# Optimization experiments

Measured on AMD Instinct MI355X. Metric: run time of the kernel, lower is better.

Reference implementation:

```python
import jax, jax.numpy as jnp
import numpy as np

SIZE, D, DLOC, NUM_LABELS = 784, 32, 2, 10
LABEL_SITE = SIZE // 2
INIT_STD = 0.01


def tree_contract(mats):
    # mats: [n, B, D, D]; binary-tree pairwise matmul matching the torch loop
    # (odd level: last matrix set aside, re-appended after the pairwise bmm)
    n = mats.shape[0]
    while n > 1:
        if n % 2 == 1:
            lone = mats[-1:]
            mats = mats[:-1]
        else:
            lone = None
        mats = jnp.einsum('nbij,nbjk->nbik', mats[0::2], mats[1::2])
        if lone is not None:
            mats = jnp.concatenate([mats, lone], axis=0)
        n = mats.shape[0]
    return mats[0]  # [B, D, D]


def setup_inputs() -> dict:
    key = jax.random.key(0)
    k1, k2, k3 = jax.random.split(key, 3)
    batch_input = jax.random.uniform(k1, (128, SIZE), dtype=jnp.float32)
    # 'random_eye' init: identity (broadcast over site / physical / label dims) + noise
    core_tensors = (jnp.broadcast_to(jnp.eye(D, dtype=jnp.float32)[None, :, :, None],
                                     (SIZE, D, D, DLOC))
                    + INIT_STD * jax.random.normal(k2, (SIZE, D, D, DLOC), dtype=jnp.float32))
    label_tensor = (jnp.broadcast_to(jnp.eye(D, dtype=jnp.float32)[:, :, None],
                                     (D, D, NUM_LABELS))
                    + INIT_STD * jax.random.normal(k3, (D, D, NUM_LABELS), dtype=jnp.float32))
    return {"batch_input": batch_input, "core_tensors": core_tensors,
            "label_tensor": label_tensor}


def reference(batch_input, core_tensors, label_tensor):
    # embed: x -> [1-x, x], shape [B, S, d]
    embedded = jnp.stack([1.0 - batch_input, batch_input], axis=-1)
    # contract each core with its local feature vector -> [S, B, D, D]
    batch_mats = jnp.einsum('sijd,bsd->sbij', core_tensors, embedded)
    left = tree_contract(batch_mats[:LABEL_SITE])    # [B, D, D]
    right = tree_contract(batch_mats[LABEL_SITE:])   # [B, D, D]
    # trace(left @ label_l @ right) per batch and label -> [B, num_labels]
    scores = jnp.einsum('bij,jkl,bki->bl', left, label_tensor, right)
    return scores
```

## Files before the change

### kernel.cpp

```cpp
#include <hip/hip_runtime.h>
#include <cstddef>


typedef short bfrag __attribute__((ext_vector_type(4)));
typedef float facc  __attribute__((ext_vector_type(4)));

#if !defined(__HIP_DEVICE_COMPILE__)
#define MFMA16(a, b, c) (c)
#elif __has_builtin(__builtin_amdgcn_mfma_f32_16x16x16bf16_1k)
#define MFMA16(a, b, c) __builtin_amdgcn_mfma_f32_16x16x16bf16_1k(a, b, c, 0, 0, 0)
#elif __has_builtin(__builtin_amdgcn_mfma_f32_16x16x16_bf16)
#define MFMA16(a, b, c) __builtin_amdgcn_mfma_f32_16x16x16_bf16(a, b, c, 0, 0, 0)
#else
#error "no 16x16x16 bf16 MFMA builtin on this target"
#endif

#define CORE2B_DWORDS (784 * 1024)

__device__ __forceinline__ short bf16h(float v) {
  unsigned u = __float_as_uint(v) + 0x8000u;
  return (short)(u >> 16);
}

#if defined(__HIP_DEVICE_COMPILE__) && __has_builtin(__builtin_amdgcn_cvt_pk_bf16_f32)
typedef __bf16 bf16x2 __attribute__((ext_vector_type(2)));
__device__ __forceinline__ bfrag packf4(float a, float b, float c, float d) {
  bf16x2 lo = __builtin_amdgcn_cvt_pk_bf16_f32(a, b);
  bf16x2 hi = __builtin_amdgcn_cvt_pk_bf16_f32(c, d);
  uint2 u = make_uint2(__builtin_bit_cast(unsigned, lo), __builtin_bit_cast(unsigned, hi));
  return __builtin_bit_cast(bfrag, u);
}
#else
__device__ __forceinline__ bfrag packf4(float a, float b, float c, float d) {
  bfrag r; r[0] = bf16h(a); r[1] = bf16h(b); r[2] = bf16h(c); r[3] = bf16h(d);
  return r;
}
#endif

__device__ __forceinline__ bfrag pack4(const facc v) {
  return packf4(v[0], v[1], v[2], v[3]);
}

__device__ __forceinline__ void split4(const float* v, bfrag& hi, bfrag& lo) {
#pragma unroll
  for (int j = 0; j < 4; ++j) {
    unsigned u = (__float_as_uint(v[j]) + 0x8000u) & 0xFFFF0000u;
    hi[j] = (short)(u >> 16);
    float lf = v[j] - __uint_as_float(u);
    lo[j] = bf16h(lf);
  }
}

__device__ __forceinline__ void fold_step(facc (&acc)[2][2], const float4 (&av)[2][2]) {
  bfrag Ahi[2][2], Alo[2][2], Bhi[2][2], Blo[2][2];
#pragma unroll
  for (int R = 0; R < 2; ++R)
#pragma unroll
    for (int H = 0; H < 2; ++H) {
      float v[4] = {av[R][H].x, av[R][H].y, av[R][H].z, av[R][H].w};
      split4(v, Ahi[R][H], Alo[R][H]);
    }
#pragma unroll
  for (int H = 0; H < 2; ++H)
#pragma unroll
    for (int c = 0; c < 2; ++c) {
      float v[4] = {acc[H][c][0], acc[H][c][1], acc[H][c][2], acc[H][c][3]};
      split4(v, Bhi[H][c], Blo[H][c]);
    }
  facc n[2][2];
#pragma unroll
  for (int R = 0; R < 2; ++R)
#pragma unroll
    for (int c = 0; c < 2; ++c) {
      facc z;
#pragma unroll
      for (int j = 0; j < 4; ++j) z[j] = 0.0f;
#pragma unroll
      for (int H = 0; H < 2; ++H) {
        z = MFMA16(Ahi[R][H], Bhi[H][c], z);
        z = MFMA16(Ahi[R][H], Blo[H][c], z);
        z = MFMA16(Alo[R][H], Bhi[H][c], z);
      }
      n[R][c] = z;
    }
#pragma unroll
  for (int R = 0; R < 2; ++R)
#pragma unroll
    for (int c = 0; c < 2; ++c) acc[R][c] = n[R][c];
}

__global__ __launch_bounds__(256) void xform_k(const float* __restrict__ core,
                                               unsigned* __restrict__ core2b) {
  const int s = blockIdx.x;
  const int tid = threadIdx.x;
  const float4* src = (const float4*)(core + (size_t)s * 2048);
  unsigned* dst = core2b + (size_t)s * 1024;
#pragma unroll
  for (int u = 0; u < 2; ++u) {
    int v = tid + 256 * u;
    float4 f = src[v];
    int i = v >> 4;
    int c = (v & 15) * 2;
    int r = i >> 4, col16 = i & 15;
    int h2 = c >> 4, cl = c & 15;
    int q = cl >> 2, j = cl & 3;
    float e0a = f.x - ((i == c) ? 1.0f : 0.0f);
    float e0b = f.z - ((i == c + 1) ? 1.0f : 0.0f);
    unsigned wa = ((unsigned)(unsigned short)bf16h(f.y - f.x) << 16) |
                  (unsigned)(unsigned short)bf16h(e0a);
    unsigned wb = ((unsigned)(unsigned short)bf16h(f.w - f.z) << 16) |
                  (unsigned)(unsigned short)bf16h(e0b);
    int idx = ((r * 2 + h2) * 64 + 16 * q + col16) * 4 + j;
    *(uint2*)(dst + idx) = make_uint2(wa, wb);
  }
}

__global__ __launch_bounds__(512, 4) void kchain(const float* __restrict__ x,
                                                 const unsigned* __restrict__ core2b,
                                                 float* __restrict__ halfbuf) {
  const int tid = threadIdx.x;
  const int lane = tid & 63;
  const int k = tid >> 6;
  const int col16 = lane & 15;
  const int q = lane >> 4;

  const int bid = blockIdx.x;
  const int chain = bid >> 1;
  const int half = bid & 1;
  const int b = chain >> 1;
  const int hside = chain & 1;

  const int t = half * 8 + k;
  const int start = (t < 8) ? 25 * t : 200 + 24 * (t - 8);
  const int len = (t < 8) ? 25 : 24;
  const int s_lo = hside * 392 + start;
  const int s_hi = s_lo + len - 1;

  __shared__ float smX[8][32 * 36];

  facc acc[2][2];
#pragma unroll
  for (int r = 0; r < 2; ++r)
#pragma unroll
    for (int c = 0; c < 2; ++c)
#pragma unroll
      for (int j = 0; j < 4; ++j)
        acc[r][c][j] = (16 * r + 4 * q + j == 16 * c + col16) ? 1.0f : 0.0f;

  const uint4* cp = (const uint4*)core2b;
  const float* xb = x + b * 784;

  for (int s = s_hi; s >= s_lo; --s) {
    uint4 raw[4];
#pragma unroll
    for (int f = 0; f < 4; ++f) raw[f] = cp[(size_t)s * 256 + f * 64 + lane];
    const float xv = xb[s];

    bfrag B[2][2];
#pragma unroll
    for (int h2 = 0; h2 < 2; ++h2)
#pragma unroll
      for (int c = 0; c < 2; ++c) B[h2][c] = pack4(acc[h2][c]);

    bfrag A[2][2];
#pragma unroll
    for (int r = 0; r < 2; ++r)
#pragma unroll
      for (int h2 = 0; h2 < 2; ++h2) {
        unsigned wd[4] = {raw[r * 2 + h2].x, raw[r * 2 + h2].y, raw[r * 2 + h2].z,
                          raw[r * 2 + h2].w};
        float e[4];
#pragma unroll
        for (int j = 0; j < 4; ++j) {
          float e0 = __uint_as_float(wd[j] << 16);
          float d = __uint_as_float(wd[j] & 0xFFFF0000u);
          e[j] = fmaf(xv, d, e0);
        }
        A[r][h2] = packf4(e[0], e[1], e[2], e[3]);
      }

#pragma unroll
    for (int r = 0; r < 2; ++r)
#pragma unroll
      for (int c = 0; c < 2; ++c) {
        acc[r][c] = MFMA16(A[r][0], B[0][c], acc[r][c]);
        acc[r][c] = MFMA16(A[r][1], B[1][c], acc[r][c]);
      }
  }

#pragma unroll
  for (int r = 0; r < 2; ++r)
#pragma unroll
    for (int c = 0; c < 2; ++c)
      *(float4*)&smX[k][(16 * c + col16) * 36 + 16 * r + 4 * q] =
          make_float4(acc[r][c][0], acc[r][c][1], acc[r][c][2], acc[r][c][3]);
  __syncthreads();

  facc a2[2][2];
#pragma unroll
  for (int r = 0; r < 2; ++r)
#pragma unroll
    for (int c = 0; c < 2; ++c)
#pragma unroll
      for (int j = 0; j < 4; ++j)
        a2[r][c][j] = (16 * r + 4 * q + j == 16 * c + col16) ? 1.0f : 0.0f;

  const int fo0 = (16 * 0 + col16) * 36 + 4 * q;
  const int fo1 = (16 * 1 + col16) * 36 + 4 * q;

  if ((k & 1) == 0) {
    float4 av[2][2];
#pragma unroll
    for (int R = 0; R < 2; ++R)
#pragma unroll
      for (int H = 0; H < 2; ++H)
        av[R][H] = *(const float4*)&smX[k][(R ? fo1 : fo0) + 16 * H];
    fold_step(a2, av);
#pragma unroll
    for (int R = 0; R < 2; ++R)
#pragma unroll
      for (int H = 0; H < 2; ++H)
        av[R][H] = *(const float4*)&smX[k + 1][(R ? fo1 : fo0) + 16 * H];
    fold_step(a2, av);
  }
  __syncthreads();
  if (k == 2 || k == 6) {
#pragma unroll
    for (int r = 0; r < 2; ++r)
#pragma unroll
      for (int c = 0; c < 2; ++c)
#pragma unroll
        for (int j = 0; j < 4; ++j)
          smX[k][(16 * r + 4 * q + j) * 36 + 16 * c + col16] = a2[r][c][j];
  }
  __syncthreads();
  if (k == 0 || k == 4) {
    float4 av[2][2];
#pragma unroll
    for (int R = 0; R < 2; ++R)
#pragma unroll
      for (int H = 0; H < 2; ++H)
        av[R][H] = *(const float4*)&smX[k + 2][(R ? fo1 : fo0) + 16 * H];
    fold_step(a2, av);
  }
  __syncthreads();
  if (k == 4) {
#pragma unroll
    for (int r = 0; r < 2; ++r)
#pragma unroll
      for (int c = 0; c < 2; ++c)
#pragma unroll
        for (int j = 0; j < 4; ++j)
          smX[4][(16 * r + 4 * q + j) * 36 + 16 * c + col16] = a2[r][c][j];
  }
  __syncthreads();
  if (k == 0) {
    float4 av[2][2];
#pragma unroll
    for (int R = 0; R < 2; ++R)
#pragma unroll
      for (int H = 0; H < 2; ++H)
        av[R][H] = *(const float4*)&smX[4][(R ? fo1 : fo0) + 16 * H];
    fold_step(a2, av);
    float* rm = halfbuf + (size_t)bid * 1024;
#pragma unroll
    for (int r = 0; r < 2; ++r)
#pragma unroll
      for (int c = 0; c < 2; ++c)
#pragma unroll
        for (int j = 0; j < 4; ++j)
          rm[(16 * r + 4 * q + j) * 32 + 16 * c + col16] = a2[r][c][j];
  }
}

__global__ __launch_bounds__(64) void gfin(const float* __restrict__ halfbuf,
                                           const float* __restrict__ label,
                                           float* __restrict__ out) {
  const int lane = threadIdx.x;
  const int b = blockIdx.x;
  const int col16 = lane & 15;
  const int q = lane >> 4;

  __shared__ float smF[1024];

  facc acc[2][2];
#pragma unroll
  for (int r = 0; r < 2; ++r)
#pragma unroll
    for (int c = 0; c < 2; ++c)
#pragma unroll
      for (int j = 0; j < 4; ++j)
        acc[r][c][j] = (16 * r + 4 * q + j == 16 * c + col16) ? 1.0f : 0.0f;

  const int slots[4] = {(2 * b + 1) * 2 + 0, (2 * b + 1) * 2 + 1,
                        (2 * b) * 2 + 0, (2 * b) * 2 + 1};
#pragma unroll
  for (int m = 0; m < 4; ++m) {
    const float* rm = halfbuf + (size_t)slots[m] * 1024;
    float4 av[2][2];
#pragma unroll
    for (int R = 0; R < 2; ++R)
#pragma unroll
      for (int H = 0; H < 2; ++H)
        av[R][H] = *(const float4*)&rm[(16 * R + col16) * 32 + 16 * H + 4 * q];
    fold_step(acc, av);
  }

#pragma unroll
  for (int r = 0; r < 2; ++r)
#pragma unroll
    for (int c = 0; c < 2; ++c)
#pragma unroll
      for (int j = 0; j < 4; ++j)
        smF[(16 * r + 4 * q + j) * 32 + 16 * c + col16] = acc[r][c][j];
  __syncthreads();

  float part[10];
#pragma unroll
  for (int l = 0; l < 10; ++l) part[l] = 0.0f;
#pragma unroll
  for (int u = 0; u < 16; ++u) {
    int e = lane + 64 * u;
    float v = smF[e];
    const float* lb = label + (size_t)e * 10;
#pragma unroll
    for (int l = 0; l < 10; ++l) part[l] += v * lb[l];
  }
#pragma unroll
  for (int l = 0; l < 10; ++l) {
#pragma unroll
    for (int o = 32; o > 0; o >>= 1) part[l] += __shfl_xor(part[l], o, 64);
  }
  if (lane == 0) {
#pragma unroll
    for (int l = 0; l < 10; ++l) out[b * 10 + l] = part[l];
  }
}

extern "C" void kernel_launch(void* const* d_in, const int* in_sizes, int n_in,
                              void* d_out, int out_size, void* d_ws, size_t ws_size,
                              hipStream_t stream) {
  const float* x = (const float*)d_in[0];
  const float* core = (const float*)d_in[1];
  const float* label = (const float*)d_in[2];
  float* out = (float*)d_out;

  unsigned* core2b = (unsigned*)d_ws;
  float* halfbuf = (float*)d_ws + CORE2B_DWORDS;

  hipLaunchKernelGGL(xform_k, dim3(784), dim3(256), 0, stream, core, core2b);
  hipLaunchKernelGGL(kchain, dim3(512), dim3(512), 0, stream, x, core2b, halfbuf);
  hipLaunchKernelGGL(gfin, dim3(128), dim3(64), 0, stream, halfbuf, label, out);
}
```

Before: 93.25 us.

## Split core matrix into E0 and D MFMA terms, scale B by x instead

The per-site matrix A = E0 + x*D is no longer rebuilt per element. The kernel issues two MFMAs per tile, one with E0 against B and one with D against x*B, so the per-element unpack, FMA and repack work on the A side is removed at the cost of twice the MFMA count. The transform kernel lays out the E0 and D halves as separate bf16 fragments, and x values are loaded once per lane and broadcast by shuffle instead of a scalar load each step. Launch bounds are raised to allow 8 blocks per CU, which may pressure registers. Rounding changes slightly because x*B is rounded to bf16.

```diff
diff --git a/kernel.cpp b/kernel.cpp
--- a/kernel.cpp
+++ b/kernel.cpp
@@ -37,10 +37,6 @@
 }
 #endif
 
-__device__ __forceinline__ bfrag pack4(const facc v) {
-  return packf4(v[0], v[1], v[2], v[3]);
-}
-
 __device__ __forceinline__ void split4(const float* v, bfrag& hi, bfrag& lo) {
 #pragma unroll
   for (int j = 0; j < 4; ++j) {
@@ -104,18 +100,20 @@
     int r = i >> 4, col16 = i & 15;
     int h2 = c >> 4, cl = c & 15;
     int q = cl >> 2, j = cl & 3;
+    int lane = col16 + 16 * q;
+    int slot = (r * 2 + h2) * 64 + lane;
     float e0a = f.x - ((i == c) ? 1.0f : 0.0f);
     float e0b = f.z - ((i == c + 1) ? 1.0f : 0.0f);
-    unsigned wa = ((unsigned)(unsigned short)bf16h(f.y - f.x) << 16) |
-                  (unsigned)(unsigned short)bf16h(e0a);
-    unsigned wb = ((unsigned)(unsigned short)bf16h(f.w - f.z) << 16) |
-                  (unsigned)(unsigned short)bf16h(e0b);
-    int idx = ((r * 2 + h2) * 64 + 16 * q + col16) * 4 + j;
-    *(uint2*)(dst + idx) = make_uint2(wa, wb);
-  }
-}
-
-__global__ __launch_bounds__(512, 4) void kchain(const float* __restrict__ x,
+    unsigned e0pair = ((unsigned)(unsigned short)bf16h(e0b) << 16) |
+                      (unsigned)(unsigned short)bf16h(e0a);
+    unsigned dpair = ((unsigned)(unsigned short)bf16h(f.w - f.z) << 16) |
+                     (unsigned)(unsigned short)bf16h(f.y - f.x);
+    dst[4 * slot + (j >> 1)] = e0pair;
+    dst[4 * slot + 2 + (j >> 1)] = dpair;
+  }
+}
+
+__global__ __launch_bounds__(512, 8) void kchain(const float* __restrict__ x,
                                                  const unsigned* __restrict__ core2b,
                                                  float* __restrict__ halfbuf) {
   const int tid = threadIdx.x;
@@ -150,41 +148,36 @@
   const uint4* cp = (const uint4*)core2b;
   const float* xb = x + b * 784;
 
+  float xr = (lane < len) ? xb[s_lo + lane] : 0.0f;
+
   for (int s = s_hi; s >= s_lo; --s) {
     uint4 raw[4];
 #pragma unroll
     for (int f = 0; f < 4; ++f) raw[f] = cp[(size_t)s * 256 + f * 64 + lane];
-    const float xv = xb[s];
-
-    bfrag B[2][2];
+    const float xv = __shfl(xr, s - s_lo, 64);
+
+    bfrag B[2][2], Bx[2][2];
 #pragma unroll
     for (int h2 = 0; h2 < 2; ++h2)
 #pragma unroll
-      for (int c = 0; c < 2; ++c) B[h2][c] = pack4(acc[h2][c]);
-
-    bfrag A[2][2];
+      for (int c = 0; c < 2; ++c) {
+        facc a = acc[h2][c];
+        B[h2][c] = packf4(a[0], a[1], a[2], a[3]);
+        Bx[h2][c] = packf4(xv * a[0], xv * a[1], xv * a[2], xv * a[3]);
+      }
+
 #pragma unroll
     for (int r = 0; r < 2; ++r)
 #pragma unroll
       for (int h2 = 0; h2 < 2; ++h2) {
-        unsigned wd[4] = {raw[r * 2 + h2].x, raw[r * 2 + h2].y, raw[r * 2 + h2].z,
-                          raw[r * 2 + h2].w};
-        float e[4];
-#pragma unroll
-        for (int j = 0; j < 4; ++j) {
-          float e0 = __uint_as_float(wd[j] << 16);
-          float d = __uint_as_float(wd[j] & 0xFFFF0000u);
-          e[j] = fmaf(xv, d, e0);
+        const uint4 rw = raw[r * 2 + h2];
+        bfrag E0 = __builtin_bit_cast(bfrag, make_uint2(rw.x, rw.y));
+        bfrag Dd = __builtin_bit_cast(bfrag, make_uint2(rw.z, rw.w));
+#pragma unroll
+        for (int c = 0; c < 2; ++c) {
+          acc[r][c] = MFMA16(Dd, Bx[h2][c], acc[r][c]);
+          acc[r][c] = MFMA16(E0, B[h2][c], acc[r][c]);
         }
-        A[r][h2] = packf4(e[0], e[1], e[2], e[3]);
-      }
-
-#pragma unroll
-    for (int r = 0; r < 2; ++r)
-#pragma unroll
-      for (int c = 0; c < 2; ++c) {
-        acc[r][c] = MFMA16(A[r][0], B[0][c], acc[r][c]);
-        acc[r][c] = MFMA16(A[r][1], B[1][c], acc[r][c]);
       }
   }
 
```

After: 97.85 us. +4.9%, slower.

## Fuse three kernels into one persistent kernel with grid barrier and last-block finalize

Applied to the files above, without the earlier changes.

Merges the core-transform, chain-contraction and final-trace kernels into one launch. A global atomic counter acts as a grid-wide barrier between the transform phase and the chain phase. A per-batch atomic counter lets the last of the four finishing blocks do the label contraction. This removes two kernel launch gaps and the separate final pass. The cost is a memset launch plus spin-waiting, and the barrier can deadlock if the 512 blocks cannot all be resident at once; a bounded guard mitigates this but may silently break correctness.

```diff
diff --git a/kernel.cpp b/kernel.cpp
--- a/kernel.cpp
+++ b/kernel.cpp
@@ -15,7 +15,16 @@
 #error "no 16x16x16 bf16 MFMA builtin on this target"
 #endif
 
+#if defined(__HIP_DEVICE_COMPILE__)
+#define S_SLEEP() __builtin_amdgcn_s_sleep(2)
+#else
+#define S_SLEEP()
+#endif
+
 #define CORE2B_DWORDS (784 * 1024)
+#define HALF_FLOATS (512 * 1024)
+#define CTR_DWORD_OFF (CORE2B_DWORDS + HALF_FLOATS)
+#define NBLK 512u
 
 __device__ __forceinline__ short bf16h(float v) {
   unsigned u = __float_as_uint(v) + 0x8000u;
@@ -89,251 +98,263 @@
     for (int c = 0; c < 2; ++c) acc[R][c] = n[R][c];
 }
 
-__global__ __launch_bounds__(256) void xform_k(const float* __restrict__ core,
-                                               unsigned* __restrict__ core2b) {
-  const int s = blockIdx.x;
+__global__ __launch_bounds__(512, 4) void fused_k(const float* __restrict__ x,
+                                                  const float* __restrict__ core,
+                                                  const float* __restrict__ label,
+                                                  unsigned* __restrict__ core2b,
+                                                  float* __restrict__ halfbuf,
+                                                  unsigned* __restrict__ ctrs,
+                                                  float* __restrict__ out) {
   const int tid = threadIdx.x;
-  const float4* src = (const float4*)(core + (size_t)s * 2048);
-  unsigned* dst = core2b + (size_t)s * 1024;
-#pragma unroll
-  for (int u = 0; u < 2; ++u) {
-    int v = tid + 256 * u;
-    float4 f = src[v];
-    int i = v >> 4;
-    int c = (v & 15) * 2;
-    int r = i >> 4, col16 = i & 15;
-    int h2 = c >> 4, cl = c & 15;
-    int q = cl >> 2, j = cl & 3;
-    float e0a = f.x - ((i == c) ? 1.0f : 0.0f);
-    float e0b = f.z - ((i == c + 1) ? 1.0f : 0.0f);
-    unsigned wa = ((unsigned)(unsigned short)bf16h(f.y - f.x) << 16) |
-                  (unsigned)(unsigned short)bf16h(e0a);
-    unsigned wb = ((unsigned)(unsigned short)bf16h(f.w - f.z) << 16) |
-                  (unsigned)(unsigned short)bf16h(e0b);
-    int idx = ((r * 2 + h2) * 64 + 16 * q + col16) * 4 + j;
-    *(uint2*)(dst + idx) = make_uint2(wa, wb);
+  const int bid = blockIdx.x;
+  __shared__ float smX[8][32 * 36];
+
+  {
+    const int gtid = bid * 512 + tid;
+    for (int idx = gtid; idx < 784 * 512; idx += 512 * 512) {
+      const int s = idx >> 9;
+      const int v = idx & 511;
+      const float4 f = ((const float4*)(core + (size_t)s * 2048))[v];
+      unsigned* dst = core2b + (size_t)s * 1024;
+      int i = v >> 4;
+      int c = (v & 15) * 2;
+      int r = i >> 4, col16 = i & 15;
+      int h2 = c >> 4, cl = c & 15;
+      int q = cl >> 2, j = cl & 3;
+      float e0a = f.x - ((i == c) ? 1.0f : 0.0f);
+      float e0b = f.z - ((i == c + 1) ? 1.0f : 0.0f);
+      unsigned wa = ((unsigned)(unsigned short)bf16h(f.y - f.x) << 16) |
+                    (unsigned)(unsigned short)bf16h(e0a);
+      unsigned wb = ((unsigned)(unsigned short)bf16h(f.w - f.z) << 16) |
+                    (unsigned)(unsigned short)bf16h(e0b);
+      int di = ((r * 2 + h2) * 64 + 16 * q + col16) * 4 + j;
+      *(uint2*)(dst + di) = make_uint2(wa, wb);
+    }
   }
-}
-
-__global__ __launch_bounds__(512, 4) void kchain(const float* __restrict__ x,
-                                                 const unsigned* __restrict__ core2b,
-                                                 float* __restrict__ halfbuf) {
-  const int tid = threadIdx.x;
-  const int lane = tid & 63;
-  const int k = tid >> 6;
-  const int col16 = lane & 15;
-  const int q = lane >> 4;
-
-  const int bid = blockIdx.x;
-  const int chain = bid >> 1;
-  const int half = bid & 1;
-  const int b = chain >> 1;
-  const int hside = chain & 1;
-
-  const int t = half * 8 + k;
-  const int start = (t < 8) ? 25 * t : 200 + 24 * (t - 8);
-  const int len = (t < 8) ? 25 : 24;
-  const int s_lo = hside * 392 + start;
-  const int s_hi = s_lo + len - 1;
-
-  __shared__ float smX[8][32 * 36];
-
-  facc acc[2][2];
-#pragma unroll
-  for (int r = 0; r < 2; ++r)
-#pragma unroll
-    for (int c = 0; c < 2; ++c)
-#pragma unroll
-      for (int j = 0; j < 4; ++j)
-        acc[r][c][j] = (16 * r + 4 * q + j == 16 * c + col16) ? 1.0f : 0.0f;
-
-  const uint4* cp = (const uint4*)core2b;
-  const float* xb = x + b * 784;
-
-  for (int s = s_hi; s >= s_lo; --s) {
-    uint4 raw[4];
-#pragma unroll
-    for (int f = 0; f < 4; ++f) raw[f] = cp[(size_t)s * 256 + f * 64 + lane];
-    const float xv = xb[s];
-
-    bfrag B[2][2];
-#pragma unroll
-    for (int h2 = 0; h2 < 2; ++h2)
-#pragma unroll
-      for (int c = 0; c < 2; ++c) B[h2][c] = pack4(acc[h2][c]);
-
-    bfrag A[2][2];
-#pragma unroll
-    for (int r = 0; r < 2; ++r)
-#pragma unroll
-      for (int h2 = 0; h2 < 2; ++h2) {
-        unsigned wd[4] = {raw[r * 2 + h2].x, raw[r * 2 + h2].y, raw[r * 2 + h2].z,
-                          raw[r * 2 + h2].w};
-        float e[4];
-#pragma unroll
-        for (int j = 0; j < 4; ++j) {
-          float e0 = __uint_as_float(wd[j] << 16);
-          float d = __uint_as_float(wd[j] & 0xFFFF0000u);
-          e[j] = fmaf(xv, d, e0);
-        }
-        A[r][h2] = packf4(e[0], e[1], e[2], e[3]);
-      }
-
-#pragma unroll
-    for (int r = 0; r < 2; ++r)
-#pragma unroll
-      for (int c = 0; c < 2; ++c) {
-        acc[r][c] = MFMA16(A[r][0], B[0][c], acc[r][c]);
-        acc[r][c] = MFMA16(A[r][1], B[1][c], acc[r][c]);
-      }
-  }
-
-#pragma unroll
-  for (int r = 0; r < 2; ++r)
-#pragma unroll
-    for (int c = 0; c < 2; ++c)
-      *(float4*)&smX[k][(16 * c + col16) * 36 + 16 * r + 4 * q] =
-          make_float4(acc[r][c][0], acc[r][c][1], acc[r][c][2], acc[r][c][3]);
+
+  __threadfence();
   __syncthreads();
-
-  facc a2[2][2];
-#pragma unroll
-  for (int r = 0; r < 2; ++r)
-#pragma unroll
-    for (int c = 0; c < 2; ++c)
-#pragma unroll
-      for (int j = 0; j < 4; ++j)
-        a2[r][c][j] = (16 * r + 4 * q + j == 16 * c + col16) ? 1.0f : 0.0f;
-
-  const int fo0 = (16 * 0 + col16) * 36 + 4 * q;
-  const int fo1 = (16 * 1 + col16) * 36 + 4 * q;
-
-  if ((k & 1) == 0) {
-    float4 av[2][2];
-#pragma unroll
-    for (int R = 0; R < 2; ++R)
-#pragma unroll
-      for (int H = 0; H < 2; ++H)
-        av[R][H] = *(const float4*)&smX[k][(R ? fo1 : fo0) + 16 * H];
-    fold_step(a2, av);
-#pragma unroll
-    for (int R = 0; R < 2; ++R)
-#pragma unroll
-      for (int H = 0; H < 2; ++H)
-        av[R][H] = *(const float4*)&smX[k + 1][(R ? fo1 : fo0) + 16 * H];
-    fold_step(a2, av);
+  if (tid == 0) {
+    __hip_atomic_fetch_add(&ctrs[0], 1u, __ATOMIC_ACQ_REL, __HIP_MEMORY_SCOPE_AGENT);
+    int guard = 0;
+    while (__hip_atomic_load(&ctrs[0], __ATOMIC_RELAXED, __HIP_MEMORY_SCOPE_AGENT) <
+           NBLK) {
+      S_SLEEP();
+      if (++guard > (1 << 22)) break;
+    }
   }
   __syncthreads();
-  if (k == 2 || k == 6) {
+  __threadfence();
+
+  {
+    const int lane = tid & 63;
+    const int k = tid >> 6;
+    const int col16 = lane & 15;
+    const int q = lane >> 4;
+
+    const int chain = bid >> 1;
+    const int half = bid & 1;
+    const int b = chain >> 1;
+    const int hside = chain & 1;
+
+    const int t = half * 8 + k;
+    const int start = (t < 8) ? 25 * t : 200 + 24 * (t - 8);
+    const int len = (t < 8) ? 25 : 24;
+    const int s_lo = hside * 392 + start;
+    const int s_hi = s_lo + len - 1;
+
+    facc acc[2][2];
 #pragma unroll
     for (int r = 0; r < 2; ++r)
 #pragma unroll
       for (int c = 0; c < 2; ++c)
 #pragma unroll
         for (int j = 0; j < 4; ++j)
-          smX[k][(16 * r + 4 * q + j) * 36 + 16 * c + col16] = a2[r][c][j];
-  }
-  __syncthreads();
-  if (k == 0 || k == 4) {
-    float4 av[2][2];
-#pragma unroll
-    for (int R = 0; R < 2; ++R)
-#pragma unroll
-      for (int H = 0; H < 2; ++H)
-        av[R][H] = *(const float4*)&smX[k + 2][(R ? fo1 : fo0) + 16 * H];
-    fold_step(a2, av);
-  }
-  __syncthreads();
-  if (k == 4) {
+          acc[r][c][j] = (16 * r + 4 * q + j == 16 * c + col16) ? 1.0f : 0.0f;
+
+    const uint4* cp = (const uint4*)core2b;
+    const float* xb = x + b * 784;
+
+    for (int s = s_hi; s >= s_lo; --s) {
+      uint4 raw[4];
+#pragma unroll
+      for (int f = 0; f < 4; ++f) raw[f] = cp[(size_t)s * 256 + f * 64 + lane];
+      const float xv = xb[s];
+
+      bfrag B[2][2];
+#pragma unroll
+      for (int h2 = 0; h2 < 2; ++h2)
+#pragma unroll
+        for (int c = 0; c < 2; ++c) B[h2][c] = pack4(acc[h2][c]);
+
+      bfrag A[2][2];
+#pragma unroll
+      for (int r = 0; r < 2; ++r)
+#pragma unroll
+        for (int h2 = 0; h2 < 2; ++h2) {
+          unsigned wd[4] = {raw[r * 2 + h2].x, raw[r * 2 + h2].y, raw[r * 2 + h2].z,
+                            raw[r * 2 + h2].w};
+          float e[4];
+#pragma unroll
+          for (int j = 0; j < 4; ++j) {
+            float e0 = __uint_as_float(wd[j] << 16);
+            float d = __uint_as_float(wd[j] & 0xFFFF0000u);
+            e[j] = fmaf(xv, d, e0);
+          }
+          A[r][h2] = packf4(e[0], e[1], e[2], e[3]);
+        }
+
+#pragma unroll
+      for (int r = 0; r < 2; ++r)
+#pragma unroll
+        for (int c = 0; c < 2; ++c) {
+          acc[r][c] = MFMA16(A[r][0], B[0][c], acc[r][c]);
+          acc[r][c] = MFMA16(A[r][1], B[1][c], acc[r][c]);
+        }
+    }
+
 #pragma unroll
     for (int r = 0; r < 2; ++r)
 #pragma unroll
       for (int c = 0; c < 2; ++c)
+        *(float4*)&smX[k][(16 * c + col16) * 36 + 16 * r + 4 * q] =
+            make_float4(acc[r][c][0], acc[r][c][1], acc[r][c][2], acc[r][c][3]);
+    __syncthreads();
+
+    facc a2[2][2];
+#pragma unroll
+    for (int r = 0; r < 2; ++r)
+#pragma unroll
+      for (int c = 0; c < 2; ++c)
 #pragma unroll
         for (int j = 0; j < 4; ++j)
-          smX[4][(16 * r + 4 * q + j) * 36 + 16 * c + col16] = a2[r][c][j];
-  }
-  __syncthreads();
-  if (k == 0) {
-    float4 av[2][2];
-#pragma unroll
-    for (int R = 0; R < 2; ++R)
-#pragma unroll
-      for (int H = 0; H < 2; ++H)
-        av[R][H] = *(const float4*)&smX[4][(R ? fo1 : fo0) + 16 * H];
-    fold_step(a2, av);
-    float* rm = halfbuf + (size_t)bid * 1024;
-#pragma unroll
-    for (int r = 0; r < 2; ++r)
-#pragma unroll
-      for (int c = 0; c < 2; ++c)
-#pragma unroll
-        for (int j = 0; j < 4; ++j)
-          rm[(16 * r + 4 * q + j) * 32 + 16 * c + col16] = a2[r][c][j];
-  }
-}
-
-__global__ __launch_bounds__(64) void gfin(const float* __restrict__ halfbuf,
-                                           const float* __restrict__ label,
-                                           float* __restrict__ out) {
-  const int lane = threadIdx.x;
-  const int b = blockIdx.x;
-  const int col16 = lane & 15;
-  const int q = lane >> 4;
-
-  __shared__ float smF[1024];
-
-  facc acc[2][2];
-#pragma unroll
-  for (int r = 0; r < 2; ++r)
-#pragma unroll
-    for (int c = 0; c < 2; ++c)
-#pragma unroll
-      for (int j = 0; j < 4; ++j)
-        acc[r][c][j] = (16 * r + 4 * q + j == 16 * c + col16) ? 1.0f : 0.0f;
-
-  const int slots[4] = {(2 * b + 1) * 2 + 0, (2 * b + 1) * 2 + 1,
-                        (2 * b) * 2 + 0, (2 * b) * 2 + 1};
-#pragma unroll
-  for (int m = 0; m < 4; ++m) {
-    const float* rm = halfbuf + (size_t)slots[m] * 1024;
-    float4 av[2][2];
-#pragma unroll
-    for (int R = 0; R < 2; ++R)
-#pragma unroll
-      for (int H = 0; H < 2; ++H)
-        av[R][H] = *(const float4*)&rm[(16 * R + col16) * 32 + 16 * H + 4 * q];
-    fold_step(acc, av);
-  }
-
-#pragma unroll
-  for (int r = 0; r < 2; ++r)
-#pragma unroll
-    for (int c = 0; c < 2; ++c)
-#pragma unroll
-      for (int j = 0; j < 4; ++j)
-        smF[(16 * r + 4 * q + j) * 32 + 16 * c + col16] = acc[r][c][j];
-  __syncthreads();
-
-  float part[10];
-#pragma unroll
-  for (int l = 0; l < 10; ++l) part[l] = 0.0f;
-#pragma unroll
-  for (int u = 0; u < 16; ++u) {
-    int e = lane + 64 * u;
-    float v = smF[e];
-    const float* lb = label + (size_t)e * 10;
-#pragma unroll
-    for (int l = 0; l < 10; ++l) part[l] += v * lb[l];
-  }
-#pragma unroll
-  for (int l = 0; l < 10; ++l) {
-#pragma unroll
-    for (int o = 32; o > 0; o >>= 1) part[l] += __shfl_xor(part[l], o, 64);
-  }
-  if (lane == 0) {
-#pragma unroll
-    for (int l = 0; l < 10; ++l) out[b * 10 + l] = part[l];
+          a2[r][c][j] = (16 * r + 4 * q + j == 16 * c + col16) ? 1.0f : 0.0f;
+
+    const int fo0 = (16 * 0 + col16) * 36 + 4 * q;
+    const int fo1 = (16 * 1 + col16) * 36 + 4 * q;
+
+    if ((k & 1) == 0) {
+      float4 av[2][2];
+#pragma unroll
+      for (int R = 0; R < 2; ++R)
+#pragma unroll
+        for (int H = 0; H < 2; ++H)
+          av[R][H] = *(const float4*)&smX[k][(R ? fo1 : fo0) + 16 * H];
+      fold_step(a2, av);
+#pragma unroll
+      for (int R = 0; R < 2; ++R)
+#pragma unroll
+        for (int H = 0; H < 2; ++H)
+          av[R][H] = *(const float4*)&smX[k + 1][(R ? fo1 : fo0) + 16 * H];
+      fold_step(a2, av);
+    }
+    __syncthreads();
+    if (k == 2 || k == 6) {
+#pragma unroll
+      for (int r = 0; r < 2; ++r)
+#pragma unroll
+        for (int c = 0; c < 2; ++c)
+#pragma unroll
+          for (int j = 0; j < 4; ++j)
+            smX[k][(16 * r + 4 * q + j) * 36 + 16 * c + col16] = a2[r][c][j];
+    }
+    __syncthreads();
+    if (k == 0 || k == 4) {
+      float4 av[2][2];
+#pragma unroll
+      for (int R = 0; R < 2; ++R)
+#pragma unroll
+        for (int H = 0; H < 2; ++H)
+          av[R][H] = *(const float4*)&smX[k + 2][(R ? fo1 : fo0) + 16 * H];
+      fold_step(a2, av);
+    }
+    __syncthreads();
+    if (k == 4) {
+#pragma unroll
+      for (int r = 0; r < 2; ++r)
+#pragma unroll
+        for (int c = 0; c < 2; ++c)
+#pragma unroll
+          for (int j = 0; j < 4; ++j)
+            smX[4][(16 * r + 4 * q + j) * 36 + 16 * c + col16] = a2[r][c][j];
+    }
+    __syncthreads();
+    if (k == 0) {
+      float4 av[2][2];
+#pragma unroll
+      for (int R = 0; R < 2; ++R)
+#pragma unroll
+        for (int H = 0; H < 2; ++H)
+          av[R][H] = *(const float4*)&smX[4][(R ? fo1 : fo0) + 16 * H];
+      fold_step(a2, av);
+      float* rm = halfbuf + (size_t)bid * 1024;
+#pragma unroll
+      for (int r = 0; r < 2; ++r)
+#pragma unroll
+        for (int c = 0; c < 2; ++c)
+#pragma unroll
+          for (int j = 0; j < 4; ++j)
+            rm[(16 * r + 4 * q + j) * 32 + 16 * c + col16] = a2[r][c][j];
+
+      __threadfence();
+      unsigned old = 0;
+      if (lane == 0)
+        old = __hip_atomic_fetch_add(&ctrs[1 + b], 1u, __ATOMIC_ACQ_REL,
+                                     __HIP_MEMORY_SCOPE_AGENT);
+      old = __shfl(old, 0, 64);
+      if (old == 3u) {
+        __threadfence();
+
+        facc hacc[2][2];
+#pragma unroll
+        for (int r = 0; r < 2; ++r)
+#pragma unroll
+          for (int c = 0; c < 2; ++c)
+#pragma unroll
+            for (int j = 0; j < 4; ++j)
+              hacc[r][c][j] = (16 * r + 4 * q + j == 16 * c + col16) ? 1.0f : 0.0f;
+
+        const int slots[4] = {(2 * b + 1) * 2 + 0, (2 * b + 1) * 2 + 1,
+                              (2 * b) * 2 + 0, (2 * b) * 2 + 1};
+#pragma unroll
+        for (int m = 0; m < 4; ++m) {
+          const float* rm2 = halfbuf + (size_t)slots[m] * 1024;
+          float4 qv[2][2];
+#pragma unroll
+          for (int R = 0; R < 2; ++R)
+#pragma unroll
+            for (int H = 0; H < 2; ++H)
+              qv[R][H] =
+                  *(const float4*)&rm2[(16 * R + col16) * 32 + 16 * H + 4 * q];
+          fold_step(hacc, qv);
+        }
+
+        float part[10];
+#pragma unroll
+        for (int l = 0; l < 10; ++l) part[l] = 0.0f;
+#pragma unroll
+        for (int r = 0; r < 2; ++r)
+#pragma unroll
+          for (int c = 0; c < 2; ++c)
+#pragma unroll
+            for (int j = 0; j < 4; ++j) {
+              float v = hacc[r][c][j];
+              const float* lb =
+                  label + (size_t)((16 * r + 4 * q + j) * 32 + 16 * c + col16) * 10;
+#pragma unroll
+              for (int l = 0; l < 10; ++l) part[l] += v * lb[l];
+            }
+#pragma unroll
+        for (int l = 0; l < 10; ++l) {
+#pragma unroll
+          for (int o = 32; o > 0; o >>= 1) part[l] += __shfl_xor(part[l], o, 64);
+        }
+        if (lane == 0) {
+#pragma unroll
+          for (int l = 0; l < 10; ++l) out[b * 10 + l] = part[l];
+        }
+      }
+    }
   }
 }
 
@@ -347,8 +368,9 @@
 
   unsigned* core2b = (unsigned*)d_ws;
   float* halfbuf = (float*)d_ws + CORE2B_DWORDS;
-
-  hipLaunchKernelGGL(xform_k, dim3(784), dim3(256), 0, stream, core, core2b);
-  hipLaunchKernelGGL(kchain, dim3(512), dim3(512), 0, stream, x, core2b, halfbuf);
-  hipLaunchKernelGGL(gfin, dim3(128), dim3(64), 0, stream, halfbuf, label, out);
-}
+  unsigned* ctrs = (unsigned*)d_ws + CTR_DWORD_OFF;
+
+  hipMemsetAsync(ctrs, 0, (1 + 128) * sizeof(unsigned), stream);
+  hipLaunchKernelGGL(fused_k, dim3(512), dim3(512), 0, stream, x, core, label,
+                     core2b, halfbuf, ctrs, out);
+}
```

New measurement: 284.1 us. 3.05x slower.

## Fuse final label contraction into chain kernel via last-block atomic counter

Applied to the files above, without the earlier changes.

Removes the separate gfin kernel launch. Each kchain block bumps a per-batch atomic counter after writing its half-chain matrix, and the fourth block to arrive folds the four partial matrices and contracts the result with the label tensor in registers. This removes one kernel launch and its dependency gap. In exchange it adds a memset launch, threadfences, and a serial tail on the last-arriving blocks.

```diff
diff --git a/kernel.cpp b/kernel.cpp
--- a/kernel.cpp
+++ b/kernel.cpp
@@ -16,6 +16,8 @@
 #endif
 
 #define CORE2B_DWORDS (784 * 1024)
+#define HALF_FLOATS (512 * 1024)
+#define CTR_DWORD_OFF (CORE2B_DWORDS + HALF_FLOATS)
 
 __device__ __forceinline__ short bf16h(float v) {
   unsigned u = __float_as_uint(v) + 0x8000u;
@@ -117,7 +119,10 @@
 
 __global__ __launch_bounds__(512, 4) void kchain(const float* __restrict__ x,
                                                  const unsigned* __restrict__ core2b,
-                                                 float* __restrict__ halfbuf) {
+                                                 float* __restrict__ halfbuf,
+                                                 unsigned* __restrict__ ctrs,
+                                                 const float* __restrict__ label,
+                                                 float* __restrict__ out) {
   const int tid = threadIdx.x;
   const int lane = tid & 63;
   const int k = tid >> 6;
@@ -270,70 +275,64 @@
 #pragma unroll
         for (int j = 0; j < 4; ++j)
           rm[(16 * r + 4 * q + j) * 32 + 16 * c + col16] = a2[r][c][j];
-  }
-}
-
-__global__ __launch_bounds__(64) void gfin(const float* __restrict__ halfbuf,
-                                           const float* __restrict__ label,
-                                           float* __restrict__ out) {
-  const int lane = threadIdx.x;
-  const int b = blockIdx.x;
-  const int col16 = lane & 15;
-  const int q = lane >> 4;
-
-  __shared__ float smF[1024];
-
-  facc acc[2][2];
-#pragma unroll
-  for (int r = 0; r < 2; ++r)
-#pragma unroll
-    for (int c = 0; c < 2; ++c)
-#pragma unroll
-      for (int j = 0; j < 4; ++j)
-        acc[r][c][j] = (16 * r + 4 * q + j == 16 * c + col16) ? 1.0f : 0.0f;
-
-  const int slots[4] = {(2 * b + 1) * 2 + 0, (2 * b + 1) * 2 + 1,
-                        (2 * b) * 2 + 0, (2 * b) * 2 + 1};
-#pragma unroll
-  for (int m = 0; m < 4; ++m) {
-    const float* rm = halfbuf + (size_t)slots[m] * 1024;
-    float4 av[2][2];
-#pragma unroll
-    for (int R = 0; R < 2; ++R)
-#pragma unroll
-      for (int H = 0; H < 2; ++H)
-        av[R][H] = *(const float4*)&rm[(16 * R + col16) * 32 + 16 * H + 4 * q];
-    fold_step(acc, av);
-  }
-
-#pragma unroll
-  for (int r = 0; r < 2; ++r)
-#pragma unroll
-    for (int c = 0; c < 2; ++c)
-#pragma unroll
-      for (int j = 0; j < 4; ++j)
-        smF[(16 * r + 4 * q + j) * 32 + 16 * c + col16] = acc[r][c][j];
-  __syncthreads();
-
-  float part[10];
-#pragma unroll
-  for (int l = 0; l < 10; ++l) part[l] = 0.0f;
-#pragma unroll
-  for (int u = 0; u < 16; ++u) {
-    int e = lane + 64 * u;
-    float v = smF[e];
-    const float* lb = label + (size_t)e * 10;
-#pragma unroll
-    for (int l = 0; l < 10; ++l) part[l] += v * lb[l];
-  }
-#pragma unroll
-  for (int l = 0; l < 10; ++l) {
-#pragma unroll
-    for (int o = 32; o > 0; o >>= 1) part[l] += __shfl_xor(part[l], o, 64);
-  }
-  if (lane == 0) {
-#pragma unroll
-    for (int l = 0; l < 10; ++l) out[b * 10 + l] = part[l];
+
+    __threadfence();
+    unsigned old = 0;
+    if (lane == 0)
+      old = __hip_atomic_fetch_add(&ctrs[b], 1u, __ATOMIC_ACQ_REL,
+                                   __HIP_MEMORY_SCOPE_AGENT);
+    old = __shfl(old, 0, 64);
+    if (old == 3u) {
+      __threadfence();
+
+      facc hacc[2][2];
+#pragma unroll
+      for (int r = 0; r < 2; ++r)
+#pragma unroll
+        for (int c = 0; c < 2; ++c)
+#pragma unroll
+          for (int j = 0; j < 4; ++j)
+            hacc[r][c][j] = (16 * r + 4 * q + j == 16 * c + col16) ? 1.0f : 0.0f;
+
+      const int slots[4] = {(2 * b + 1) * 2 + 0, (2 * b + 1) * 2 + 1,
+                            (2 * b) * 2 + 0, (2 * b) * 2 + 1};
+#pragma unroll
+      for (int m = 0; m < 4; ++m) {
+        const float* rm2 = halfbuf + (size_t)slots[m] * 1024;
+        float4 qv[2][2];
+#pragma unroll
+        for (int R = 0; R < 2; ++R)
+#pragma unroll
+          for (int H = 0; H < 2; ++H)
+            qv[R][H] = *(const float4*)&rm2[(16 * R + col16) * 32 + 16 * H + 4 * q];
+        fold_step(hacc, qv);
+      }
+
+      float part[10];
+#pragma unroll
+      for (int l = 0; l < 10; ++l) part[l] = 0.0f;
+#pragma unroll
+      for (int r = 0; r < 2; ++r)
+#pragma unroll
+        for (int c = 0; c < 2; ++c)
+#pragma unroll
+          for (int j = 0; j < 4; ++j) {
+            float v = hacc[r][c][j];
+            const float* lb =
+                label + (size_t)((16 * r + 4 * q + j) * 32 + 16 * c + col16) * 10;
+#pragma unroll
+            for (int l = 0; l < 10; ++l) part[l] += v * lb[l];
+          }
+#pragma unroll
+      for (int l = 0; l < 10; ++l) {
+#pragma unroll
+        for (int o = 32; o > 0; o >>= 1) part[l] += __shfl_xor(part[l], o, 64);
+      }
+      if (lane == 0) {
+#pragma unroll
+        for (int l = 0; l < 10; ++l) out[b * 10 + l] = part[l];
+      }
+    }
   }
 }
 
@@ -347,8 +346,10 @@
 
   unsigned* core2b = (unsigned*)d_ws;
   float* halfbuf = (float*)d_ws + CORE2B_DWORDS;
-
+  unsigned* ctrs = (unsigned*)d_ws + CTR_DWORD_OFF;
+
+  hipMemsetAsync(ctrs, 0, 128 * sizeof(unsigned), stream);
   hipLaunchKernelGGL(xform_k, dim3(784), dim3(256), 0, stream, core, core2b);
-  hipLaunchKernelGGL(kchain, dim3(512), dim3(512), 0, stream, x, core2b, halfbuf);
-  hipLaunchKernelGGL(gfin, dim3(128), dim3(64), 0, stream, halfbuf, label, out);
-}
+  hipLaunchKernelGGL(kchain, dim3(512), dim3(512), 0, stream, x, core2b, halfbuf,
+                     ctrs, label, out);
+}
```

After: 120.2 us. 1.29x slower.
